# Performance work log

Measured on AMD Instinct MI355X. Metric: run time of the kernel, lower is better.

The kernel has to match this reference:

```python
import jax, jax.numpy as jnp
import numpy as np

B, S, D, H = 2, 2048, 1024, 16
AD = D // H  # per-head dim = 64


def setup_inputs() -> dict:
    key = jax.random.key(0)
    k1, k2, k3 = jax.random.split(key, 3)
    x = jax.random.normal(k1, (B, S, D), dtype=jnp.float32)
    W_qkv = jax.random.normal(k2, (D, 3 * D), dtype=jnp.float32) * (1.0 / np.sqrt(D))
    b_qkv = jax.random.normal(k3, (3 * D,), dtype=jnp.float32) * 0.01
    return {"x": x, "W_qkv": W_qkv, "b_qkv": b_qkv}


def reference(x, W_qkv, b_qkv):
    b, s, _ = x.shape
    qkv = x @ W_qkv + b_qkv                      # [B,S,3D]
    qkv = qkv.reshape(b, s, H, 3 * AD)           # per-head interleaved qkv
    qkv = jnp.transpose(qkv, (0, 2, 1, 3))       # [B,H,S,3*ad]
    q = qkv[..., :AD]
    k = qkv[..., AD:2 * AD]
    v = qkv[..., 2 * AD:]
    scale = 1.0 / jnp.sqrt(jnp.asarray(AD, dtype=x.dtype))
    att = jnp.einsum("bhqd,bhkd->bhqk", q, k) * scale  # [B,H,S,S]
    att = jax.nn.softmax(att, axis=-1)
    values = jnp.einsum("bhqk,bhkd->bhqd", att, v)     # [B,H,S,ad]
    # Faithful to source: reshape [B,H,S,ad] -> [B,S,ad*H] WITHOUT head transpose
    return values.reshape(b, s, AD * H)
```

## Files before the change

### kernel.cpp

```cpp
#include <hip/hip_runtime.h>
#include <stdint.h>
#include <stddef.h>

#define S_LEN 2048
#define NH 16
#define HD 64
#define DM 1024
#define NQKV 3072
#define MROWS 4096
#define NBH 32

typedef float f32x4 __attribute__((ext_vector_type(4)));
typedef __bf16 bf16x8 __attribute__((ext_vector_type(8)));
typedef __bf16 bf16x4 __attribute__((ext_vector_type(4)));
typedef short short8_t __attribute__((ext_vector_type(8)));

__device__ __forceinline__ unsigned short f2bf(float f) {
  union { float f; unsigned int u; } v; v.f = f;
  unsigned int u = v.u;
  u += 0x7FFFu + ((u >> 16) & 1u);
  return (unsigned short)(u >> 16);
}

__device__ __forceinline__ void async_copy16(const void* g, void* l) {
  __builtin_amdgcn_global_load_lds(
      (const __attribute__((address_space(1))) void*)g,
      (__attribute__((address_space(3))) void*)l, 16, 0, 0);
}

#define WAITCNT_BARRIER(N)                                          \
  asm volatile("s_waitcnt vmcnt(" #N ")" ::: "memory");             \
  __builtin_amdgcn_sched_barrier(0);                                \
  __builtin_amdgcn_s_barrier();                                     \
  __builtin_amdgcn_sched_barrier(0);

__global__ __launch_bounds__(256) void cast_x_kernel(const float* __restrict__ x,
                                                     unsigned short* __restrict__ xb) {
  size_t i = ((size_t)blockIdx.x * 256 + threadIdx.x) * 8;
  f32x4 a = *(const f32x4*)(x + i);
  f32x4 b = *(const f32x4*)(x + i + 4);
  union { unsigned short u[8]; short8_t v; } o;
  o.u[0] = f2bf(a[0]); o.u[1] = f2bf(a[1]); o.u[2] = f2bf(a[2]); o.u[3] = f2bf(a[3]);
  o.u[4] = f2bf(b[0]); o.u[5] = f2bf(b[1]); o.u[6] = f2bf(b[2]); o.u[7] = f2bf(b[3]);
  *(short8_t*)(xb + i) = o.v;
}

__global__ __launch_bounds__(256) void transpose_w_kernel(const float* __restrict__ W,
                                                          unsigned short* __restrict__ wt) {
  __shared__ float tile[32][33];
  const int n0 = blockIdx.x * 32;
  const int k0 = blockIdx.y * 32;
  const int tx = threadIdx.x;
  const int ty = threadIdx.y;
  #pragma unroll
  for (int i = 0; i < 4; ++i)
    tile[ty + i * 8][tx] = W[(size_t)(k0 + ty + i * 8) * NQKV + n0 + tx];
  __syncthreads();
  #pragma unroll
  for (int i = 0; i < 4; ++i)
    wt[(size_t)(n0 + ty + i * 8) * DM + k0 + tx] = f2bf(tile[tx][ty + i * 8]);
}

__global__ __launch_bounds__(256) void qkv_gemm_kernel(
    const unsigned short* __restrict__ xb, const unsigned short* __restrict__ wt,
    const float* __restrict__ bias,
    unsigned short* __restrict__ Qb, unsigned short* __restrict__ Kb,
    unsigned short* __restrict__ Vt) {
  __shared__ __align__(16) unsigned char Sh[4][128 * 64 * 2];
  const int t = threadIdx.x;
  const int lane = t & 63;
  const int wave = t >> 6;
  const int wm = (wave >> 1) * 64, wn = (wave & 1) * 64;
  const int lr = lane & 15, g = lane >> 4;
  const int m0 = blockIdx.x * 128, n0 = blockIdx.y * 128;

  f32x4 acc[4][4];
  #pragma unroll
  for (int i = 0; i < 4; ++i)
    #pragma unroll
    for (int j = 0; j < 4; ++j) acc[i][j] = f32x4{0.f, 0.f, 0.f, 0.f};

  auto stage = [&](int kt, int buf) __attribute__((always_inline)) {
    const int k0 = kt * 64;
    #pragma unroll
    for (int i = 0; i < 4; ++i) {
      int c = t + i * 256;
      int row = c >> 3;
      int cc = (c & 7) ^ (row & 7);
      async_copy16(xb + (size_t)(m0 + row) * DM + k0 + cc * 8, Sh[buf * 2] + c * 16);
      async_copy16(wt + (size_t)(n0 + row) * DM + k0 + cc * 8, Sh[buf * 2 + 1] + c * 16);
    }
  };

  auto compute = [&](int buf) __attribute__((always_inline)) {
    unsigned char* const As = Sh[buf * 2];
    unsigned char* const Bs = Sh[buf * 2 + 1];
    bf16x8 af[2][4], bfr[2][4];
    #pragma unroll
    for (int kk = 0; kk < 2; ++kk) {
      #pragma unroll
      for (int i = 0; i < 4; ++i) {
        int ra = wm + i * 16 + lr;
        af[kk][i] = *(const bf16x8*)(As + ((ra * 128 + kk * 64 + g * 16) ^ ((ra & 7) << 4)));
        int rb = wn + i * 16 + lr;
        bfr[kk][i] = *(const bf16x8*)(Bs + ((rb * 128 + kk * 64 + g * 16) ^ ((rb & 7) << 4)));
      }
    }
    __builtin_amdgcn_s_setprio(1);
    #pragma unroll
    for (int kk = 0; kk < 2; ++kk)
      #pragma unroll
      for (int mi = 0; mi < 4; ++mi)
        #pragma unroll
        for (int ni = 0; ni < 4; ++ni)
          acc[mi][ni] = __builtin_amdgcn_mfma_f32_16x16x32_bf16(
              af[kk][mi], bfr[kk][ni], acc[mi][ni], 0, 0, 0);
    __builtin_amdgcn_s_setprio(0);
  };

  stage(0, 0);
  __syncthreads();
  for (int kt = 0; kt < DM / 64; kt += 2) {
    stage(kt + 1, 1);
    compute(0);
    __syncthreads();
    if (kt + 2 < DM / 64) stage(kt + 2, 0);
    compute(1);
    __syncthreads();
  }

  const float QSC = 0.18033688011112042f;
  const int nbase = n0 + wn;
  const int h = nbase / 192;
  const int typ = (nbase % 192) >> 6;
  const int b = m0 >> 11;
  const int bh = b * NH + h;

  if (typ == 2) {
    unsigned char* const T = Sh[0] + wave * 8192;
    #pragma unroll
    for (int ni = 0; ni < 4; ++ni) {
      int col = ni * 16 + lr;
      float bv = bias[nbase + col];
      #pragma unroll
      for (int mi = 0; mi < 4; ++mi) {
        bf16x4 w;
        w[0] = (__bf16)(acc[mi][ni][0] + bv);
        w[1] = (__bf16)(acc[mi][ni][1] + bv);
        w[2] = (__bf16)(acc[mi][ni][2] + bv);
        w[3] = (__bf16)(acc[mi][ni][3] + bv);
        int byte = (col * 128 + (mi * 16 + g * 4) * 2) ^ ((col & 7) << 4);
        *(bf16x4*)(T + byte) = w;
      }
    }
    asm volatile("s_waitcnt lgkmcnt(0)" ::: "memory");
    __builtin_amdgcn_sched_barrier(0);
    const int s0 = (m0 & 2047) + wm + (lane & 7) * 8;
    #pragma unroll
    for (int i = 0; i < 8; ++i) {
      int col = i * 8 + (lane >> 3);
      int byte = (col * 128 + (lane & 7) * 16) ^ ((col & 7) << 4);
      bf16x8 v = *(const bf16x8*)(T + byte);
      *(bf16x8*)(Vt + ((size_t)bh * HD + col) * S_LEN + s0) = v;
    }
  } else {
    unsigned short* const dst = (typ == 0) ? Qb : Kb;
    const float sc = (typ == 0) ? QSC : 1.0f;
    #pragma unroll
    for (int ni = 0; ni < 4; ++ni) {
      int d = ni * 16 + lr;
      float bv = bias[nbase + d];
      #pragma unroll
      for (int mi = 0; mi < 4; ++mi) {
        #pragma unroll
        for (int r = 0; r < 4; ++r) {
          int s = (m0 & 2047) + wm + mi * 16 + g * 4 + r;
          dst[((size_t)bh * S_LEN + s) * HD + d] = f2bf((acc[mi][ni][r] + bv) * sc);
        }
      }
    }
  }
}

__global__ __launch_bounds__(512) void attn_kernel(
    const unsigned short* __restrict__ Qb, const unsigned short* __restrict__ Kb,
    const unsigned short* __restrict__ Vt, float* __restrict__ out) {
  __shared__ __align__(16) unsigned char smem[81920];
  const int t = threadIdx.x;
  const int lane = t & 63;
  const int wave = t >> 6;
  const int lr = lane & 15, g = lane >> 4;
  const int bh = blockIdx.y;
  const int q0 = blockIdx.x * 128 + wave * 16;

  const unsigned short* Qbh = Qb + (size_t)bh * S_LEN * HD;
  const unsigned short* Kbh = Kb + (size_t)bh * S_LEN * HD;
  const unsigned short* Vbh = Vt + (size_t)bh * HD * S_LEN;

  bf16x8 qf[2];
  #pragma unroll
  for (int kk = 0; kk < 2; ++kk)
    qf[kk] = *(const bf16x8*)(Qbh + (size_t)(q0 + lr) * HD + kk * 32 + g * 8);

  union { unsigned short u[8]; bf16x8 v; } one_c;
  #pragma unroll
  for (int j = 0; j < 8; ++j) one_c.u[j] = 0x3F80;
  const bf16x8 ones8 = one_c.v;

  int kvOff[4][2];
  #pragma unroll
  for (int i = 0; i < 4; ++i)
    #pragma unroll
    for (int kk = 0; kk < 2; ++kk) {
      int r = i * 16 + lr;
      kvOff[i][kk] = (r * 128 + kk * 64 + g * 16) ^ ((r & 7) << 4);
    }
  unsigned char* const Pw = smem + 65536 + wave * 2048;
  int pWr[4];
  #pragma unroll
  for (int ni = 0; ni < 4; ++ni)
    pWr[ni] = (lr * 128 + ni * 32 + g * 8) ^ ((lr & 7) << 4);

  const int c0 = t;
  const int row0 = c0 >> 3;
  const int cc0 = (c0 & 7) ^ (row0 & 7);
  const int kGO0 = row0 * HD + cc0 * 8;
  const int vGO0 = row0 * S_LEN + cc0 * 8;

  f32x4 lacc = f32x4{0.f, 0.f, 0.f, 0.f};
  f32x4 oacc[4];
  #pragma unroll
  for (int di = 0; di < 4; ++di) oacc[di] = f32x4{0.f, 0.f, 0.f, 0.f};

  auto stage = [&](int kt, int buf) __attribute__((always_inline)) {
    const unsigned short* kp = Kbh + (size_t)kt * (64 * HD);
    const unsigned short* vp = Vbh + kt * 64;
    unsigned char* const base = smem + buf * 16384;
    async_copy16(kp + kGO0, base + c0 * 16);
    async_copy16(vp + vGO0, base + 8192 + c0 * 16);
  };

  auto compute = [&](int buf) __attribute__((always_inline)) {
    unsigned char* const Ksb = smem + buf * 16384;
    unsigned char* const Vsb = Ksb + 8192;
    f32x4 sacc[4];
    #pragma unroll
    for (int ni = 0; ni < 4; ++ni) sacc[ni] = f32x4{-8.f, -8.f, -8.f, -8.f};
    __builtin_amdgcn_s_setprio(1);
    #pragma unroll
    for (int ni = 0; ni < 4; ++ni)
      #pragma unroll
      for (int kk = 0; kk < 2; ++kk) {
        bf16x8 kf = *(const bf16x8*)(Ksb + kvOff[ni][kk]);
        sacc[ni] = __builtin_amdgcn_mfma_f32_16x16x32_bf16(kf, qf[kk], sacc[ni], 0, 0, 0);
      }
    __builtin_amdgcn_s_setprio(0);

    #pragma unroll
    for (int ni = 0; ni < 4; ++ni) {
      bf16x4 w;
      w[0] = (__bf16)exp2f(sacc[ni][0]);
      w[1] = (__bf16)exp2f(sacc[ni][1]);
      w[2] = (__bf16)exp2f(sacc[ni][2]);
      w[3] = (__bf16)exp2f(sacc[ni][3]);
      *(bf16x4*)(Pw + pWr[ni]) = w;
    }

    bf16x8 pf[2];
    #pragma unroll
    for (int kk = 0; kk < 2; ++kk)
      pf[kk] = *(const bf16x8*)(Pw + kvOff[0][kk]);
    __builtin_amdgcn_s_setprio(1);
    #pragma unroll
    for (int di = 0; di < 4; ++di)
      #pragma unroll
      for (int kk = 0; kk < 2; ++kk) {
        bf16x8 vf = *(const bf16x8*)(Vsb + kvOff[di][kk]);
        oacc[di] = __builtin_amdgcn_mfma_f32_16x16x32_bf16(vf, pf[kk], oacc[di], 0, 0, 0);
      }
    #pragma unroll
    for (int kk = 0; kk < 2; ++kk)
      lacc = __builtin_amdgcn_mfma_f32_16x16x32_bf16(ones8, pf[kk], lacc, 0, 0, 0);
    __builtin_amdgcn_s_setprio(0);
  };

  stage(0, 0);
  stage(1, 1);
  for (int kt4 = 0; kt4 < 28; kt4 += 4) {
    stage(kt4 + 2, 2); WAITCNT_BARRIER(4); compute(0);
    stage(kt4 + 3, 3); WAITCNT_BARRIER(4); compute(1);
    stage(kt4 + 4, 0); WAITCNT_BARRIER(4); compute(2);
    stage(kt4 + 5, 1); WAITCNT_BARRIER(4); compute(3);
  }
  stage(30, 2); WAITCNT_BARRIER(4); compute(0);
  stage(31, 3); WAITCNT_BARRIER(4); compute(1);
  WAITCNT_BARRIER(2); compute(2);
  WAITCNT_BARRIER(0); compute(3);

  float inv = 1.0f / lacc[0];
  float* outp = out + ((size_t)bh * S_LEN + q0 + lr) * HD;
  #pragma unroll
  for (int di = 0; di < 4; ++di) {
    f32x4 o = oacc[di] * inv;
    *(f32x4*)(outp + di * 16 + g * 4) = o;
  }
}

extern "C" void kernel_launch(void* const* d_in, const int* in_sizes, int n_in,
                              void* d_out, int out_size, void* d_ws, size_t ws_size,
                              hipStream_t stream) {
  const float* x    = (const float*)d_in[0];
  const float* W    = (const float*)d_in[1];
  const float* bias = (const float*)d_in[2];
  float* out = (float*)d_out;

  unsigned short* xb = (unsigned short*)d_ws;
  unsigned short* wt = xb + (size_t)MROWS * DM;
  unsigned short* Qb = wt + (size_t)NQKV * DM;
  unsigned short* Kb = Qb + (size_t)NBH * S_LEN * HD;
  unsigned short* Vt = Kb + (size_t)NBH * S_LEN * HD;

  cast_x_kernel<<<(MROWS * DM) / (256 * 8), 256, 0, stream>>>(x, xb);
  transpose_w_kernel<<<dim3(NQKV / 32, DM / 32), dim3(32, 8), 0, stream>>>(W, wt);
  qkv_gemm_kernel<<<dim3(MROWS / 128, NQKV / 128), 256, 0, stream>>>(xb, wt, bias, Qb, Kb, Vt);
  attn_kernel<<<dim3(S_LEN / 128, NBH), 512, 0, stream>>>(Qb, Kb, Vt, out);
}
```

Measured before the change: 96.24 us.

## Switch attention to 32x32x16 MFMA with in-register P via permlane32 swap

Rewrites the attention inner loop to use 32x32x16 bf16 MFMA, with 4 waves of 32 query rows each instead of 8 waves of 16 rows. The exp'd probabilities are rearranged in registers with v_permlane32_swap instead of a round trip through LDS, which removes the P scratch buffer and its LDS traffic. Each block now stages twice as many K/V chunks per thread, and the wait counts are adjusted to match. The cost is higher register pressure from the 16-wide accumulators. The score init offset of -8 is dropped, so the exp2 outputs are no longer shifted, which may affect overflow safety.

```diff
diff --git a/kernel.cpp b/kernel.cpp
--- a/kernel.cpp
+++ b/kernel.cpp
@@ -11,9 +11,12 @@
 #define NBH 32
 
 typedef float f32x4 __attribute__((ext_vector_type(4)));
+typedef float f32x16 __attribute__((ext_vector_type(16)));
 typedef __bf16 bf16x8 __attribute__((ext_vector_type(8)));
 typedef __bf16 bf16x4 __attribute__((ext_vector_type(4)));
+typedef __bf16 bf16x2v __attribute__((ext_vector_type(2)));
 typedef short short8_t __attribute__((ext_vector_type(8)));
+typedef unsigned int u32x4 __attribute__((ext_vector_type(4)));
 
 __device__ __forceinline__ unsigned short f2bf(float f) {
   union { float f; unsigned int u; } v; v.f = f;
@@ -182,127 +185,135 @@
   }
 }
 
-__global__ __launch_bounds__(512) void attn_kernel(
+__global__ __launch_bounds__(256, 2) void attn_kernel(
     const unsigned short* __restrict__ Qb, const unsigned short* __restrict__ Kb,
     const unsigned short* __restrict__ Vt, float* __restrict__ out) {
-  __shared__ __align__(16) unsigned char smem[81920];
+  __shared__ __align__(16) unsigned char smem[65536];
   const int t = threadIdx.x;
   const int lane = t & 63;
   const int wave = t >> 6;
-  const int lr = lane & 15, g = lane >> 4;
+  const int l5 = lane & 31, hi = lane >> 5;
   const int bh = blockIdx.y;
-  const int q0 = blockIdx.x * 128 + wave * 16;
-
-  const unsigned short* Qbh = Qb + (size_t)bh * S_LEN * HD;
+  const int q0 = blockIdx.x * 128 + wave * 32;
+
   const unsigned short* Kbh = Kb + (size_t)bh * S_LEN * HD;
   const unsigned short* Vbh = Vt + (size_t)bh * HD * S_LEN;
 
-  bf16x8 qf[2];
-  #pragma unroll
-  for (int kk = 0; kk < 2; ++kk)
-    qf[kk] = *(const bf16x8*)(Qbh + (size_t)(q0 + lr) * HD + kk * 32 + g * 8);
+  const unsigned short* Qrow = Qb + ((size_t)bh * S_LEN + q0 + l5) * HD;
+  bf16x8 qf[4];
+  #pragma unroll
+  for (int ks = 0; ks < 4; ++ks)
+    qf[ks] = *(const bf16x8*)(Qrow + ks * 16 + hi * 8);
 
   union { unsigned short u[8]; bf16x8 v; } one_c;
   #pragma unroll
   for (int j = 0; j < 8; ++j) one_c.u[j] = 0x3F80;
   const bf16x8 ones8 = one_c.v;
 
-  int kvOff[4][2];
-  #pragma unroll
-  for (int i = 0; i < 4; ++i)
-    #pragma unroll
-    for (int kk = 0; kk < 2; ++kk) {
-      int r = i * 16 + lr;
-      kvOff[i][kk] = (r * 128 + kk * 64 + g * 16) ^ ((r & 7) << 4);
-    }
-  unsigned char* const Pw = smem + 65536 + wave * 2048;
-  int pWr[4];
-  #pragma unroll
-  for (int ni = 0; ni < 4; ++ni)
-    pWr[ni] = (lr * 128 + ni * 32 + g * 8) ^ ((lr & 7) << 4);
-
-  const int c0 = t;
-  const int row0 = c0 >> 3;
-  const int cc0 = (c0 & 7) ^ (row0 & 7);
-  const int kGO0 = row0 * HD + cc0 * 8;
-  const int vGO0 = row0 * S_LEN + cc0 * 8;
-
-  f32x4 lacc = f32x4{0.f, 0.f, 0.f, 0.f};
-  f32x4 oacc[4];
-  #pragma unroll
-  for (int di = 0; di < 4; ++di) oacc[di] = f32x4{0.f, 0.f, 0.f, 0.f};
+  int kvOff[2][4];
+  #pragma unroll
+  for (int rb = 0; rb < 2; ++rb)
+    #pragma unroll
+    for (int ks = 0; ks < 4; ++ks) {
+      int r = rb * 32 + l5;
+      kvOff[rb][ks] = (r * 128 + ks * 32 + hi * 16) ^ ((l5 & 7) << 4);
+    }
+
+  const int c0 = t, c1 = t + 256;
+  const int row0 = c0 >> 3, row1 = c1 >> 3;
+  const int cc0 = (c0 & 7) ^ (row0 & 7), cc1 = (c1 & 7) ^ (row1 & 7);
+  const int kGO0 = row0 * HD + cc0 * 8, kGO1 = row1 * HD + cc1 * 8;
+  const int vGO0 = row0 * S_LEN + cc0 * 8, vGO1 = row1 * S_LEN + cc1 * 8;
+
+  f32x16 oacc0, oacc1, lacc;
+  #pragma unroll
+  for (int i = 0; i < 16; ++i) { oacc0[i] = 0.f; oacc1[i] = 0.f; lacc[i] = 0.f; }
 
   auto stage = [&](int kt, int buf) __attribute__((always_inline)) {
     const unsigned short* kp = Kbh + (size_t)kt * (64 * HD);
     const unsigned short* vp = Vbh + kt * 64;
     unsigned char* const base = smem + buf * 16384;
     async_copy16(kp + kGO0, base + c0 * 16);
+    async_copy16(kp + kGO1, base + c1 * 16);
     async_copy16(vp + vGO0, base + 8192 + c0 * 16);
+    async_copy16(vp + vGO1, base + 8192 + c1 * 16);
   };
 
   auto compute = [&](int buf) __attribute__((always_inline)) {
     unsigned char* const Ksb = smem + buf * 16384;
     unsigned char* const Vsb = Ksb + 8192;
-    f32x4 sacc[4];
-    #pragma unroll
-    for (int ni = 0; ni < 4; ++ni) sacc[ni] = f32x4{-8.f, -8.f, -8.f, -8.f};
+
+    f32x16 sacc0, sacc1;
+    #pragma unroll
+    for (int i = 0; i < 16; ++i) { sacc0[i] = 0.f; sacc1[i] = 0.f; }
     __builtin_amdgcn_s_setprio(1);
     #pragma unroll
-    for (int ni = 0; ni < 4; ++ni)
-      #pragma unroll
-      for (int kk = 0; kk < 2; ++kk) {
-        bf16x8 kf = *(const bf16x8*)(Ksb + kvOff[ni][kk]);
-        sacc[ni] = __builtin_amdgcn_mfma_f32_16x16x32_bf16(kf, qf[kk], sacc[ni], 0, 0, 0);
-      }
+    for (int ks = 0; ks < 4; ++ks) {
+      bf16x8 kf0 = *(const bf16x8*)(Ksb + kvOff[0][ks]);
+      sacc0 = __builtin_amdgcn_mfma_f32_32x32x16_bf16(kf0, qf[ks], sacc0, 0, 0, 0);
+      bf16x8 kf1 = *(const bf16x8*)(Ksb + kvOff[1][ks]);
+      sacc1 = __builtin_amdgcn_mfma_f32_32x32x16_bf16(kf1, qf[ks], sacc1, 0, 0, 0);
+    }
     __builtin_amdgcn_s_setprio(0);
 
-    #pragma unroll
-    for (int ni = 0; ni < 4; ++ni) {
-      bf16x4 w;
-      w[0] = (__bf16)exp2f(sacc[ni][0]);
-      w[1] = (__bf16)exp2f(sacc[ni][1]);
-      w[2] = (__bf16)exp2f(sacc[ni][2]);
-      w[3] = (__bf16)exp2f(sacc[ni][3]);
-      *(bf16x4*)(Pw + pWr[ni]) = w;
-    }
-
-    bf16x8 pf[2];
-    #pragma unroll
-    for (int kk = 0; kk < 2; ++kk)
-      pf[kk] = *(const bf16x8*)(Pw + kvOff[0][kk]);
+    unsigned wv0[8], wv1[8];
+    #pragma unroll
+    for (int rr = 0; rr < 8; ++rr) {
+      bf16x2v ca;
+      ca[0] = (__bf16)exp2f(sacc0[2 * rr]);
+      ca[1] = (__bf16)exp2f(sacc0[2 * rr + 1]);
+      wv0[rr] = __builtin_bit_cast(unsigned, ca);
+      bf16x2v cb;
+      cb[0] = (__bf16)exp2f(sacc1[2 * rr]);
+      cb[1] = (__bf16)exp2f(sacc1[2 * rr + 1]);
+      wv1[rr] = __builtin_bit_cast(unsigned, cb);
+    }
+
     __builtin_amdgcn_s_setprio(1);
     #pragma unroll
-    for (int di = 0; di < 4; ++di)
-      #pragma unroll
-      for (int kk = 0; kk < 2; ++kk) {
-        bf16x8 vf = *(const bf16x8*)(Vsb + kvOff[di][kk]);
-        oacc[di] = __builtin_amdgcn_mfma_f32_16x16x32_bf16(vf, pf[kk], oacc[di], 0, 0, 0);
-      }
-    #pragma unroll
-    for (int kk = 0; kk < 2; ++kk)
-      lacc = __builtin_amdgcn_mfma_f32_16x16x32_bf16(ones8, pf[kk], lacc, 0, 0, 0);
+    for (int kstep = 0; kstep < 4; ++kstep) {
+      const int kkl = kstep & 1;
+      unsigned a0, a1, b0, b1;
+      if (kstep < 2) { a0 = wv0[4 * kkl]; a1 = wv0[4 * kkl + 1]; b0 = wv0[4 * kkl + 2]; b1 = wv0[4 * kkl + 3]; }
+      else           { a0 = wv1[4 * kkl]; a1 = wv1[4 * kkl + 1]; b0 = wv1[4 * kkl + 2]; b1 = wv1[4 * kkl + 3]; }
+      asm("v_permlane32_swap_b32 %0, %1" : "+v"(a0), "+v"(b0));
+      asm("v_permlane32_swap_b32 %0, %1" : "+v"(a1), "+v"(b1));
+      u32x4 tmp; tmp[0] = a0; tmp[1] = a1; tmp[2] = b0; tmp[3] = b1;
+      bf16x8 pf = __builtin_bit_cast(bf16x8, tmp);
+      bf16x8 vf0 = *(const bf16x8*)(Vsb + kvOff[0][kstep]);
+      oacc0 = __builtin_amdgcn_mfma_f32_32x32x16_bf16(vf0, pf, oacc0, 0, 0, 0);
+      bf16x8 vf1 = *(const bf16x8*)(Vsb + kvOff[1][kstep]);
+      oacc1 = __builtin_amdgcn_mfma_f32_32x32x16_bf16(vf1, pf, oacc1, 0, 0, 0);
+      lacc = __builtin_amdgcn_mfma_f32_32x32x16_bf16(ones8, pf, lacc, 0, 0, 0);
+    }
     __builtin_amdgcn_s_setprio(0);
   };
 
   stage(0, 0);
   stage(1, 1);
   for (int kt4 = 0; kt4 < 28; kt4 += 4) {
-    stage(kt4 + 2, 2); WAITCNT_BARRIER(4); compute(0);
-    stage(kt4 + 3, 3); WAITCNT_BARRIER(4); compute(1);
-    stage(kt4 + 4, 0); WAITCNT_BARRIER(4); compute(2);
-    stage(kt4 + 5, 1); WAITCNT_BARRIER(4); compute(3);
+    stage(kt4 + 2, 2); WAITCNT_BARRIER(8); compute(0);
+    stage(kt4 + 3, 3); WAITCNT_BARRIER(8); compute(1);
+    stage(kt4 + 4, 0); WAITCNT_BARRIER(8); compute(2);
+    stage(kt4 + 5, 1); WAITCNT_BARRIER(8); compute(3);
   }
-  stage(30, 2); WAITCNT_BARRIER(4); compute(0);
-  stage(31, 3); WAITCNT_BARRIER(4); compute(1);
-  WAITCNT_BARRIER(2); compute(2);
+  stage(30, 2); WAITCNT_BARRIER(8); compute(0);
+  stage(31, 3); WAITCNT_BARRIER(8); compute(1);
+  WAITCNT_BARRIER(4); compute(2);
   WAITCNT_BARRIER(0); compute(3);
 
   float inv = 1.0f / lacc[0];
-  float* outp = out + ((size_t)bh * S_LEN + q0 + lr) * HD;
-  #pragma unroll
-  for (int di = 0; di < 4; ++di) {
-    f32x4 o = oacc[di] * inv;
-    *(f32x4*)(outp + di * 16 + g * 4) = o;
+  float* outp = out + ((size_t)bh * S_LEN + q0 + l5) * HD;
+  #pragma unroll
+  for (int b = 0; b < 4; ++b) {
+    f32x4 o0, o1;
+    #pragma unroll
+    for (int j = 0; j < 4; ++j) {
+      o0[j] = oacc0[b * 4 + j] * inv;
+      o1[j] = oacc1[b * 4 + j] * inv;
+    }
+    *(f32x4*)(outp + b * 8 + hi * 4) = o0;
+    *(f32x4*)(outp + 32 + b * 8 + hi * 4) = o1;
   }
 }
 
@@ -323,5 +334,5 @@
   cast_x_kernel<<<(MROWS * DM) / (256 * 8), 256, 0, stream>>>(x, xb);
   transpose_w_kernel<<<dim3(NQKV / 32, DM / 32), dim3(32, 8), 0, stream>>>(W, wt);
   qkv_gemm_kernel<<<dim3(MROWS / 128, NQKV / 128), 256, 0, stream>>>(xb, wt, bias, Qb, Kb, Vt);
-  attn_kernel<<<dim3(S_LEN / 128, NBH), 512, 0, stream>>>(Qb, Kb, Vt, out);
-}
+  attn_kernel<<<dim3(S_LEN / 128, NBH), 256, 0, stream>>>(Qb, Kb, Vt, out);
+}
```

After: 99.20 us. 1.03x slower.

## Pipeline QKV GEMM with four-stage K=32 LDS ring and counted waits

Applied to the files above, without the earlier changes.

The QKV projection GEMM switches from a double-buffered K=64 pipeline that calls __syncthreads after every tile to a four-buffer ring of K=32 tiles. Loads are issued two stages ahead, and each step uses WAITCNT_BARRIER(4) so the newest copies can stay in flight while the current tile is consumed. LDS swizzle offsets are precomputed once outside the loop. This aims to hide global-load latency and reduce barrier stalls, but it doubles the number of barriers and leaves only 16 MFMAs per step.

```diff
diff --git a/kernel.cpp b/kernel.cpp
--- a/kernel.cpp
+++ b/kernel.cpp
@@ -66,7 +66,7 @@
     const float* __restrict__ bias,
     unsigned short* __restrict__ Qb, unsigned short* __restrict__ Kb,
     unsigned short* __restrict__ Vt) {
-  __shared__ __align__(16) unsigned char Sh[4][128 * 64 * 2];
+  __shared__ __align__(16) unsigned char Sh[65536];
   const int t = threadIdx.x;
   const int lane = t & 63;
   const int wave = t >> 6;
@@ -80,54 +80,60 @@
     #pragma unroll
     for (int j = 0; j < 4; ++j) acc[i][j] = f32x4{0.f, 0.f, 0.f, 0.f};
 
+  const int c0 = t, c1 = t + 256;
+  const int row0 = c0 >> 2, row1 = c1 >> 2;
+  const int ap0 = ((c0 & 3) ^ (row0 & 3)) * 8, ap1 = ((c1 & 3) ^ (row1 & 3)) * 8;
+
   auto stage = [&](int kt, int buf) __attribute__((always_inline)) {
-    const int k0 = kt * 64;
+    const int k0 = kt * 32;
+    unsigned char* const base = Sh + buf * 16384;
+    async_copy16(xb + (size_t)(m0 + row0) * DM + k0 + ap0, base + c0 * 16);
+    async_copy16(xb + (size_t)(m0 + row1) * DM + k0 + ap1, base + c1 * 16);
+    async_copy16(wt + (size_t)(n0 + row0) * DM + k0 + ap0, base + 8192 + c0 * 16);
+    async_copy16(wt + (size_t)(n0 + row1) * DM + k0 + ap1, base + 8192 + c1 * 16);
+  };
+
+  int aOff[4], bOff[4];
+  #pragma unroll
+  for (int i = 0; i < 4; ++i) {
+    int ra = wm + i * 16 + lr;
+    aOff[i] = ra * 64 + ((g ^ (ra & 3)) << 4);
+    int rb = wn + i * 16 + lr;
+    bOff[i] = 8192 + rb * 64 + ((g ^ (rb & 3)) << 4);
+  }
+
+  auto compute = [&](int buf) __attribute__((always_inline)) {
+    unsigned char* const base = Sh + buf * 16384;
+    bf16x8 af[4], bfr[4];
     #pragma unroll
     for (int i = 0; i < 4; ++i) {
-      int c = t + i * 256;
-      int row = c >> 3;
-      int cc = (c & 7) ^ (row & 7);
-      async_copy16(xb + (size_t)(m0 + row) * DM + k0 + cc * 8, Sh[buf * 2] + c * 16);
-      async_copy16(wt + (size_t)(n0 + row) * DM + k0 + cc * 8, Sh[buf * 2 + 1] + c * 16);
-    }
-  };
-
-  auto compute = [&](int buf) __attribute__((always_inline)) {
-    unsigned char* const As = Sh[buf * 2];
-    unsigned char* const Bs = Sh[buf * 2 + 1];
-    bf16x8 af[2][4], bfr[2][4];
-    #pragma unroll
-    for (int kk = 0; kk < 2; ++kk) {
-      #pragma unroll
-      for (int i = 0; i < 4; ++i) {
-        int ra = wm + i * 16 + lr;
-        af[kk][i] = *(const bf16x8*)(As + ((ra * 128 + kk * 64 + g * 16) ^ ((ra & 7) << 4)));
-        int rb = wn + i * 16 + lr;
-        bfr[kk][i] = *(const bf16x8*)(Bs + ((rb * 128 + kk * 64 + g * 16) ^ ((rb & 7) << 4)));
-      }
+      af[i] = *(const bf16x8*)(base + aOff[i]);
+      bfr[i] = *(const bf16x8*)(base + bOff[i]);
     }
     __builtin_amdgcn_s_setprio(1);
     #pragma unroll
-    for (int kk = 0; kk < 2; ++kk)
-      #pragma unroll
-      for (int mi = 0; mi < 4; ++mi)
-        #pragma unroll
-        for (int ni = 0; ni < 4; ++ni)
-          acc[mi][ni] = __builtin_amdgcn_mfma_f32_16x16x32_bf16(
-              af[kk][mi], bfr[kk][ni], acc[mi][ni], 0, 0, 0);
+    for (int mi = 0; mi < 4; ++mi)
+      #pragma unroll
+      for (int ni = 0; ni < 4; ++ni)
+        acc[mi][ni] = __builtin_amdgcn_mfma_f32_16x16x32_bf16(
+            af[mi], bfr[ni], acc[mi][ni], 0, 0, 0);
     __builtin_amdgcn_s_setprio(0);
   };
 
   stage(0, 0);
+  stage(1, 1);
+  for (int t4 = 0; t4 < 28; t4 += 4) {
+    WAITCNT_BARRIER(4); stage(t4 + 2, 2); compute(0);
+    WAITCNT_BARRIER(4); stage(t4 + 3, 3); compute(1);
+    WAITCNT_BARRIER(4); stage(t4 + 4, 0); compute(2);
+    WAITCNT_BARRIER(4); stage(t4 + 5, 1); compute(3);
+  }
+  WAITCNT_BARRIER(4); stage(30, 2); compute(0);
+  WAITCNT_BARRIER(4); stage(31, 3); compute(1);
+  WAITCNT_BARRIER(4); compute(2);
+  WAITCNT_BARRIER(0); compute(3);
+
   __syncthreads();
-  for (int kt = 0; kt < DM / 64; kt += 2) {
-    stage(kt + 1, 1);
-    compute(0);
-    __syncthreads();
-    if (kt + 2 < DM / 64) stage(kt + 2, 0);
-    compute(1);
-    __syncthreads();
-  }
 
   const float QSC = 0.18033688011112042f;
   const int nbase = n0 + wn;
@@ -137,7 +143,7 @@
   const int bh = b * NH + h;
 
   if (typ == 2) {
-    unsigned char* const T = Sh[0] + wave * 8192;
+    unsigned char* const T = Sh + wave * 8192;
     #pragma unroll
     for (int ni = 0; ni < 4; ++ni) {
       int col = ni * 16 + lr;
```

Result: slower. 100.1 us (+4.1%).
